# Optimization experiments

Measured on AMD Instinct MI355X. Metric: run time of the kernel, lower is better.

The kernel has to match this reference:

```python
import jax, jax.numpy as jnp
import numpy as np


def setup_inputs() -> dict:
    key = jax.random.key(0)
    ks = jax.random.split(key, 12)
    C, H, L, P = 256, 8, 4, 4
    Lq, Lx = 2048, 300
    iss = jnp.array([[64, 64], [32, 32], [16, 16], [8, 8]], dtype=jnp.int32)
    Len_in = int(np.sum(np.array(iss)[:, 0] * np.array(iss)[:, 1]))  # 5440
    lsi = jnp.array([0, 4096, 5120, 5376], dtype=jnp.int32)
    return {
        "query": jax.random.normal(ks[0], (1, Lq, C), jnp.float32),
        "reference_points": jax.random.uniform(ks[1], (1, Lq, L, 2), jnp.float32),
        "input_flatten": jax.random.normal(ks[2], (1, Len_in, C), jnp.float32),
        "input_spatial_shapes": iss,
        "add_keys": jax.random.normal(ks[3], (1, Lx, C), jnp.float32),
        "input_level_start_index": lsi,
        "W_off": jax.random.normal(ks[4], (H * L * P * 2, C), jnp.float32) * 0.01,
        "b_off": jax.random.normal(ks[5], (H * L * P * 2,), jnp.float32),
        "W_attn": jax.random.normal(ks[6], (H * (L + 1), C, C), jnp.float32) * 0.05,
        "W_v": jax.random.normal(ks[7], (H * 2, C, C), jnp.float32) * 0.05,
        "b_v": jax.random.normal(ks[8], (H * 2, C), jnp.float32) * 0.01,
        "W_mix": jax.random.normal(ks[9], (C, H + 1), jnp.float32) * 0.5,
    }


def reference(query, reference_points, input_flatten, input_spatial_shapes,
              add_keys, input_level_start_index, W_off, b_off, W_attn, W_v, b_v, W_mix):
    N, Lq, C = query.shape
    L = input_spatial_shapes.shape[0]
    H = W_v.shape[0] // 2
    P = W_off.shape[0] // (H * L * 2)

    # sampling locations: ref (x,y in [0,1]) + offsets / (W,H)
    off = (query @ W_off.T + b_off).reshape(N, Lq, H, L, P, 2)
    wh = input_spatial_shapes[:, ::-1].astype(query.dtype)  # (L,2) = (W,H)
    loc = reference_points[:, :, None, :, None, :] + off / wh[None, None, None, :, None, :]

    # get_keys: truncating index computation + gather (faithful to original)
    loc = jnp.clip(loc, 0.0, 0.999)
    iss_f = input_spatial_shapes.astype(loc.dtype)[None, None, None, :, None, :]
    idx = (loc * iss_f).astype(jnp.int32)  # (N,Lq,H,L,P,2): (int(x*H_l), int(y*W_l))
    lin = (idx[..., 0]
           + idx[..., 1] * input_spatial_shapes[:, 0].astype(jnp.int32)[None, None, None, :, None]
           + input_level_start_index.astype(jnp.int32)[None, None, None, :, None])
    keys = input_flatten[0][lin[0]]                # (Lq,H,L,P,C)
    keys = jnp.transpose(keys, (1, 2, 3, 0, 4))    # (H,L,P,Lq,C)

    head_w = jax.nn.softmax(W_mix.T, axis=0)       # (H+1,C)
    qf = query[0]                                  # (Lq,C)
    ak = add_keys[0]                               # (Lx,C)

    # per-head, per-level similarity (replicates original overlapping index h*L+lvl)
    Ws = W_attn[jnp.arange(H)[:, None] * L + jnp.arange(L)[None, :]]  # (H,L,C,C)
    T = jnp.einsum('hlce,hlpqe->hlcpq', Ws, keys)  # (H,L,C,P,Lq)
    # faithful reshape quirk: (C, P*Lq) viewed as (P, Lq, C)
    T = T.reshape(H, L, P, Lq, C)
    attn_s = jnp.einsum('hlpqc,qc->hlpq', T, qf).reshape(H, L * P, Lq)

    Wadd = W_attn[jnp.arange(H) * L + L]           # (H,C,C)
    attn_a = jnp.einsum('xe,hce,qc->hxq', ak, Wadd, qf)  # (H,Lx,Lq)

    attn = jax.nn.softmax(jnp.concatenate([attn_s, attn_a], axis=1), axis=1)
    attn_s_sm, attn_a_sm = attn[:, :L * P], attn[:, L * P:]

    Wv0, bv0 = W_v[0::2], b_v[0::2]
    Wv1, bv1 = W_v[1::2], b_v[1::2]
    vals = (jnp.einsum('hlpqe,hce->hlpqc', keys, Wv0)
            + bv0[:, None, None, None, :]).reshape(H, L * P, Lq, C)
    v2 = jnp.einsum('xe,hce->hxc', ak, Wv1) + bv1[:, None, :]  # (H,Lx,C)

    out_h = (jnp.einsum('hkq,hkqc->hqc', attn_s_sm, vals)
             + jnp.einsum('hxq,hxc->hqc', attn_a_sm, v2))      # (H,Lq,C)
    result = qf * head_w[-1][None, :] + jnp.einsum('hqc,hc->qc', out_h, head_w[:-1])
    return result[None]
```

## Files before the change

### kernel.cpp

```cpp
#include <hip/hip_runtime.h>
#include <stdint.h>

#define NJ 316

typedef __attribute__((ext_vector_type(8))) short short8;
typedef __attribute__((ext_vector_type(4))) float f32x4;
union U4S8 { uint4 u; short8 s; };

__device__ __forceinline__ unsigned short f2bf(float x) {
    unsigned int u = __float_as_uint(x);
    u += 0x7fff + ((u >> 16) & 1);
    return (unsigned short)(u >> 16);
}
__device__ __forceinline__ float bf2f(unsigned short h) {
    return __uint_as_float(((unsigned int)h) << 16);
}

__global__ __launch_bounds__(256) void cvt_kernel(
    const float* __restrict__ src, unsigned short* __restrict__ dh,
    unsigned short* __restrict__ dl, int n4)
{
    for (int i = blockIdx.x * 256 + threadIdx.x; i < n4; i += gridDim.x * 256) {
        float4 v = ((const float4*)src)[i];
        unsigned short h[4], l[4];
        float x[4] = {v.x, v.y, v.z, v.w};
        #pragma unroll
        for (int j = 0; j < 4; ++j) {
            h[j] = f2bf(x[j]);
            l[j] = f2bf(x[j] - bf2f(h[j]));
        }
        ((uint2*)dh)[i] = make_uint2((unsigned)h[0] | ((unsigned)h[1] << 16),
                                     (unsigned)h[2] | ((unsigned)h[3] << 16));
        ((uint2*)dl)[i] = make_uint2((unsigned)l[0] | ((unsigned)l[1] << 16),
                                     (unsigned)l[2] | ((unsigned)l[3] << 16));
    }
}

__global__ __launch_bounds__(256) void cvt_pack_kernel(
    const float* __restrict__ src, unsigned int* __restrict__ dst, int n4)
{
    for (int i = blockIdx.x * 256 + threadIdx.x; i < n4; i += gridDim.x * 256) {
        float4 v = ((const float4*)src)[i];
        float x[4] = {v.x, v.y, v.z, v.w};
        unsigned int o[4];
        #pragma unroll
        for (int j = 0; j < 4; ++j) {
            unsigned short h = f2bf(x[j]);
            unsigned short l = f2bf(x[j] - bf2f(h));
            o[j] = (unsigned)h | ((unsigned)l << 16);
        }
        ((uint4*)dst)[i] = make_uint4(o[0], o[1], o[2], o[3]);
    }
}

__global__ __launch_bounds__(256) void cvt_wadd_kernel(
    const float* __restrict__ Wattn, unsigned short* __restrict__ dh,
    unsigned short* __restrict__ dl)
{
    int i = blockIdx.x * 256 + threadIdx.x;
    int z = i >> 16, r = i & 65535;
    float v = Wattn[(size_t)(4 * z + 4) * 65536 + r];
    unsigned short h = f2bf(v);
    dh[i] = h;
    dl[i] = f2bf(v - bf2f(h));
}

__global__ __launch_bounds__(256) void cvt_akT_kernel(
    const float* __restrict__ ak, unsigned short* __restrict__ dh,
    unsigned short* __restrict__ dl)
{
    const int e = blockIdx.x;
    for (int k = threadIdx.x; k < 320; k += 256) {
        float v = (k >= 16 && k < 316) ? ak[(k - 16) * 256 + e] : 0.f;
        unsigned short h = f2bf(v);
        dh[e * 320 + k] = h;
        dl[e * 320 + k] = f2bf(v - bf2f(h));
    }
}

__global__ __launch_bounds__(256) void lin_kernel(
    const float* __restrict__ query, const float* __restrict__ refp,
    const int* __restrict__ iss, const int* __restrict__ lsi,
    const float* __restrict__ Woff, const float* __restrict__ boff,
    int* __restrict__ lin)
{
    __shared__ float qf8[8][256];
    __shared__ float wtile[256][33];
    __shared__ double offl[8][256];
    const int t = threadIdx.x;
    const int qbase = blockIdx.x * 8;
    #pragma unroll
    for (int i = 0; i < 8; ++i) qf8[i][t] = query[(qbase + i) * 256 + t];
    double acc[8];
    #pragma unroll
    for (int r = 0; r < 8; ++r) acc[r] = 0.0;
    for (int cb = 0; cb < 256; cb += 32) {
        __syncthreads();
        #pragma unroll
        for (int i = 0; i < 32; ++i) {
            int f = i * 256 + t;
            int o = f >> 5, jj = f & 31;
            wtile[o][jj] = Woff[o * 256 + cb + jj];
        }
        __syncthreads();
        #pragma unroll
        for (int jj = 0; jj < 32; ++jj) {
            double wv = (double)wtile[t][jj];
            #pragma unroll
            for (int r = 0; r < 8; ++r)
                acc[r] += (double)qf8[r][cb + jj] * wv;
        }
    }
    double bo = (double)boff[t];
    __syncthreads();
    #pragma unroll
    for (int r = 0; r < 8; ++r) offl[r][t] = acc[r] + bo;
    __syncthreads();
    #pragma unroll
    for (int rep = 0; rep < 4; ++rep) {
        int idx = rep * 256 + t;
        int r = idx >> 7;
        int s = idx & 127;
        int l = (s >> 2) & 3;
        int q = qbase + r;
        double offx = offl[r][2 * s];
        double offy = offl[r][2 * s + 1];
        int w0 = iss[l * 2 + 0];
        int w1 = iss[l * 2 + 1];
        double locx = (double)refp[q * 8 + l * 2 + 0] + offx / (double)w1;
        double locy = (double)refp[q * 8 + l * 2 + 1] + offy / (double)w0;
        locx = fmin(fmax(locx, 0.0), 0.999);
        locy = fmin(fmax(locy, 0.0), 0.999);
        int ix = (int)(locx * (double)w0);
        int iy = (int)(locy * (double)w1);
        lin[q * 128 + s] = ix + iy * w0 + lsi[l];
    }
}

__global__ __launch_bounds__(256, 2) void gattn_mfma(
    const unsigned short* __restrict__ qh, const unsigned short* __restrict__ ql,
    const unsigned int* __restrict__ inflatP, const float* __restrict__ Wattn,
    const int* __restrict__ lin, float* __restrict__ attn)
{
    __shared__ int linrow[256];
    __shared__ float Glds[64][268];
    const int t = threadIdx.x;
    const int lane = t & 63, w = t >> 6;
    const int b = blockIdx.x;
    const int qb = b & 7, p = (b >> 3) & 3, l = (b >> 5) & 3, h = b >> 7;
    linrow[t] = lin[(256 * qb + t) * 128 + h * 16 + l * 4 + p];
    __syncthreads();

    const int l15 = lane & 15, g = lane >> 4;
    const int q2l = qb + 8 * p + 32 * l15;
    const int ebase = 64 * w + l15;

    f32x4 acc[4][4];
    #pragma unroll
    for (int i = 0; i < 4; ++i)
        #pragma unroll
        for (int eg = 0; eg < 4; ++eg) acc[i][eg] = (f32x4){0.f, 0.f, 0.f, 0.f};

    for (int kb = 0; kb < 256; kb += 32) {
        U4S8 ah[4], al[4];
        #pragma unroll
        for (int i = 0; i < 4; ++i) {
            size_t off = (size_t)(q2l + 512 * i) * 256 + kb + 8 * g;
            ah[i].u = *(const uint4*)(qh + off);
            al[i].u = *(const uint4*)(ql + off);
        }
        int rowoff[8];
        #pragma unroll
        for (int m = 0; m < 8; ++m) rowoff[m] = linrow[kb + 8 * g + m] * 256;
        unsigned int uv[4][8];
        #pragma unroll
        for (int eg = 0; eg < 4; ++eg)
            #pragma unroll
            for (int m = 0; m < 8; ++m)
                uv[eg][m] = inflatP[rowoff[m] + ebase + 16 * eg];

        #pragma unroll
        for (int eg = 0; eg < 4; ++eg) {
            U4S8 bh, bl;
            unsigned int hh[4], ll[4];
            #pragma unroll
            for (int d = 0; d < 4; ++d) {
                hh[d] = __builtin_amdgcn_perm(uv[eg][2 * d + 1], uv[eg][2 * d],
                                              0x05040100u);
                ll[d] = __builtin_amdgcn_perm(uv[eg][2 * d + 1], uv[eg][2 * d],
                                              0x07060302u);
            }
            bh.u = make_uint4(hh[0], hh[1], hh[2], hh[3]);
            bl.u = make_uint4(ll[0], ll[1], ll[2], ll[3]);
            #pragma unroll
            for (int i = 0; i < 4; ++i) {
                acc[i][eg] = __builtin_amdgcn_mfma_f32_16x16x32_bf16(
                    ah[i].s, bh.s, acc[i][eg], 0, 0, 0);
                acc[i][eg] = __builtin_amdgcn_mfma_f32_16x16x32_bf16(
                    ah[i].s, bl.s, acc[i][eg], 0, 0, 0);
                acc[i][eg] = __builtin_amdgcn_mfma_f32_16x16x32_bf16(
                    al[i].s, bh.s, acc[i][eg], 0, 0, 0);
            }
        }
    }

    #pragma unroll
    for (int i = 0; i < 4; ++i)
        #pragma unroll
        for (int eg = 0; eg < 4; ++eg)
            #pragma unroll
            for (int r = 0; r < 4; ++r)
                Glds[16 * i + 4 * g + r][64 * w + 16 * eg + l15] = acc[i][eg][r];
    __syncthreads();

    const int tx = t & 15, ty = t >> 4;
    const float* Wsbase = Wattn + (size_t)(h * 4 + l) * 65536;
    float gv[4][16];
    #pragma unroll
    for (int r = 0; r < 4; ++r)
        #pragma unroll
        for (int i2 = 0; i2 < 4; ++i2) {
            float4 gd = *(const float4*)&Glds[ty * 4 + r][tx * 4 + 64 * i2];
            gv[r][i2 * 4 + 0] = gd.x;
            gv[r][i2 * 4 + 1] = gd.y;
            gv[r][i2 * 4 + 2] = gd.z;
            gv[r][i2 * 4 + 3] = gd.w;
        }
    #pragma unroll
    for (int r = 0; r < 4; ++r) {
        int hi = ty * 4 + r;
        int q2 = qb + 8 * p + 32 * hi;
        #pragma unroll
        for (int p2 = 0; p2 < 4; ++p2) {
            const float* wr = Wsbase + (size_t)(hi + 64 * p2) * 256;
            float partial = 0.f;
            #pragma unroll
            for (int i2 = 0; i2 < 4; ++i2) {
                float4 wv = *(const float4*)&wr[tx * 4 + 64 * i2];
                partial += wv.x * gv[r][i2 * 4 + 0] + wv.y * gv[r][i2 * 4 + 1]
                         + wv.z * gv[r][i2 * 4 + 2] + wv.w * gv[r][i2 * 4 + 3];
            }
            partial += __shfl_xor(partial, 1);
            partial += __shfl_xor(partial, 2);
            partial += __shfl_xor(partial, 4);
            partial += __shfl_xor(partial, 8);
            if (tx == 0)
                attn[((size_t)h * 2048 + q2) * NJ + (l * 4 + p2)] = partial;
        }
    }
}

struct Seg {
    const unsigned short *Ah, *Al, *Bh, *Bl;
    int K, lda, ldb;
    long sA, sB;
};

template<bool ACCUM, bool OUTF32, int NSEG>
__global__ __launch_bounds__(256) void mfma_gemm(
    Seg s0, Seg s1,
    float* __restrict__ Cf, unsigned short* __restrict__ Ch,
    unsigned short* __restrict__ Cl,
    int M, int N, int ldc, long sC)
{
    __shared__ unsigned short As[2][64 * 40];
    __shared__ unsigned short Bs[2][128 * 40];
    const int t = threadIdx.x;
    const int lane = t & 63;
    const int wave = t >> 6;
    const int wm = (wave & 1) * 32, wn = (wave >> 1) * 64;
    const int nb = blockIdx.x * 128, mb = blockIdx.y * 64;
    const int z = blockIdx.z;

    f32x4 acc[2][4];
    #pragma unroll
    for (int i = 0; i < 2; ++i)
        #pragma unroll
        for (int j = 0; j < 4; ++j) acc[i][j] = (f32x4){0.f, 0.f, 0.f, 0.f};

    const int arow = t >> 2, akoff = (t & 3) * 8;
    const int frow = lane & 15, fk = (lane >> 4) * 8;

    #pragma unroll
    for (int seg = 0; seg < NSEG; ++seg) {
        const Seg S = seg ? s1 : s0;
        const unsigned short* Azh = S.Ah + (size_t)z * S.sA;
        const unsigned short* Azl = S.Al + (size_t)z * S.sA;
        const unsigned short* Bzh = S.Bh + (size_t)z * S.sB;
        const unsigned short* Bzl = S.Bl + (size_t)z * S.sB;
        for (int kb = 0; kb < S.K; kb += 32) {
            __syncthreads();
            {
                int gm = mb + arow;
                uint4 vh = {0, 0, 0, 0}, vl = {0, 0, 0, 0};
                if (gm < M) {
                    size_t o = (size_t)gm * S.lda + kb + akoff;
                    vh = *(const uint4*)(Azh + o);
                    vl = *(const uint4*)(Azl + o);
                }
                *(uint4*)&As[0][arow * 40 + akoff] = vh;
                *(uint4*)&As[1][arow * 40 + akoff] = vl;
                #pragma unroll
                for (int i = 0; i < 2; ++i) {
                    int f = i * 256 + t;
                    int brow = f >> 2, bkoff = (f & 3) * 8;
                    int gn = nb + brow;
                    uint4 wh = {0, 0, 0, 0}, wl = {0, 0, 0, 0};
                    if (gn < N) {
                        size_t o = (size_t)gn * S.ldb + kb + bkoff;
                        wh = *(const uint4*)(Bzh + o);
                        wl = *(const uint4*)(Bzl + o);
                    }
                    *(uint4*)&Bs[0][brow * 40 + bkoff] = wh;
                    *(uint4*)&Bs[1][brow * 40 + bkoff] = wl;
                }
            }
            __syncthreads();
            short8 a[2][2], b[4][2];
            #pragma unroll
            for (int i = 0; i < 2; ++i) {
                int r = wm + i * 16 + frow;
                a[i][0] = *(const short8*)&As[0][r * 40 + fk];
                a[i][1] = *(const short8*)&As[1][r * 40 + fk];
            }
            #pragma unroll
            for (int j = 0; j < 4; ++j) {
                int r = wn + j * 16 + frow;
                b[j][0] = *(const short8*)&Bs[0][r * 40 + fk];
                b[j][1] = *(const short8*)&Bs[1][r * 40 + fk];
            }
            #pragma unroll
            for (int i = 0; i < 2; ++i)
                #pragma unroll
                for (int j = 0; j < 4; ++j) {
                    acc[i][j] = __builtin_amdgcn_mfma_f32_16x16x32_bf16(
                        a[i][0], b[j][0], acc[i][j], 0, 0, 0);
                    acc[i][j] = __builtin_amdgcn_mfma_f32_16x16x32_bf16(
                        a[i][0], b[j][1], acc[i][j], 0, 0, 0);
                    acc[i][j] = __builtin_amdgcn_mfma_f32_16x16x32_bf16(
                        a[i][1], b[j][0], acc[i][j], 0, 0, 0);
                }
        }
    }
    #pragma unroll
    for (int i = 0; i < 2; ++i)
        #pragma unroll
        for (int r = 0; r < 4; ++r) {
            int gm = mb + wm + i * 16 + (lane >> 4) * 4 + r;
            if (gm >= M) continue;
            #pragma unroll
            for (int j = 0; j < 4; ++j) {
                int gn = nb + wn + j * 16 + (lane & 15);
                if (gn >= N) continue;
                size_t idx = (size_t)z * sC + (size_t)gm * ldc + gn;
                float v = acc[i][j][r];
                if (OUTF32) {
                    float prev = ACCUM ? Cf[idx] : 0.f;
                    Cf[idx] = prev + v;
                } else {
                    unsigned short h = f2bf(v);
                    Ch[idx] = h;
                    Cl[idx] = f2bf(v - bf2f(h));
                }
            }
        }
}

__global__ __launch_bounds__(256) void softmax_kernel(
    float* __restrict__ attn, float* __restrict__ s0,
    unsigned short* __restrict__ awh, unsigned short* __restrict__ awl)
{
    const int t = threadIdx.x;
    const int w = t >> 6, lane = t & 63;
    const int rid = blockIdx.x * 4 + w;
    float* row = attn + (size_t)rid * NJ;
    float v[5];
    float m = -1e30f;
    #pragma unroll
    for (int i = 0; i < 5; ++i) {
        int j = lane + 64 * i;
        v[i] = (j < NJ) ? row[j] : -1e30f;
        m = fmaxf(m, v[i]);
    }
    #pragma unroll
    for (int d = 1; d < 64; d <<= 1) m = fmaxf(m, __shfl_xor(m, d));
    float s = 0.f, sfirst = 0.f;
    #pragma unroll
    for (int i = 0; i < 5; ++i) {
        int j = lane + 64 * i;
        float e = (j < NJ) ? expf(v[i] - m) : 0.f;
        v[i] = e;
        s += e;
        if (i == 0 && lane < 16) sfirst += e;
    }
    #pragma unroll
    for (int d = 1; d < 64; d <<= 1) s += __shfl_xor(s, d);
    #pragma unroll
    for (int d = 1; d < 64; d <<= 1) sfirst += __shfl_xor(sfirst, d);
    float inv = 1.f / s;
    #pragma unroll
    for (int i = 0; i < 5; ++i) {
        int j = lane + 64 * i;
        float val = (j < NJ) ? v[i] * inv : 0.f;
        if (j < 16) row[j] = val;
        unsigned short h = f2bf(val);
        awh[(size_t)rid * 320 + j] = h;
        awl[(size_t)rid * 320 + j] = f2bf(val - bf2f(h));
    }
    if (lane == 0) s0[rid] = sfirst * inv;
}

__global__ __launch_bounds__(256) void ka_kernel(
    const float* __restrict__ inflat, const float* __restrict__ attn,
    const int* __restrict__ lin, unsigned short* __restrict__ KAh,
    unsigned short* __restrict__ KAl)
{
    __shared__ float wls[16];
    __shared__ int lls[16];
    const int b = blockIdx.x;
    const int h = b >> 11, q = b & 2047;
    const int t = threadIdx.x;
    if (t < 16) {
        wls[t] = attn[(size_t)b * NJ + t];
        lls[t] = lin[q * 128 + h * 16 + t];
    }
    __syncthreads();
    float acc = 0.f;
    #pragma unroll
    for (int k = 0; k < 16; ++k)
        acc += wls[k] * inflat[lls[k] * 256 + t];
    unsigned short hh = f2bf(acc);
    KAh[(size_t)b * 256 + t] = hh;
    KAl[(size_t)b * 256 + t] = f2bf(acc - bf2f(hh));
}

__global__ __launch_bounds__(256) void final_kernel(
    const float* __restrict__ qf, const float* __restrict__ OH,
    const float* __restrict__ s0, const float* __restrict__ bv,
    const float* __restrict__ Wmix, float* __restrict__ out)
{
    const int q = blockIdx.x, c = threadIdx.x;
    float wj[9], m = -1e30f;
    #pragma unroll
    for (int j = 0; j < 9; ++j) { wj[j] = Wmix[c * 9 + j]; m = fmaxf(m, wj[j]); }
    float s = 0.f;
    #pragma unroll
    for (int j = 0; j < 9; ++j) { wj[j] = expf(wj[j] - m); s += wj[j]; }
    float inv = 1.f / s;
    float acc = qf[q * 256 + c] * wj[8] * inv;
    #pragma unroll
    for (int h = 0; h < 8; ++h) {
        float s0v = s0[h * 2048 + q];
        float oh = OH[((size_t)h * 2048 + q) * 256 + c]
                 + s0v * bv[(2 * h) * 256 + c]
                 + (1.f - s0v) * bv[(2 * h + 1) * 256 + c];
        acc += oh * wj[h] * inv;
    }
    out[q * 256 + c] = acc;
}

extern "C" void kernel_launch(void* const* d_in, const int* in_sizes, int n_in,
                              void* d_out, int out_size, void* d_ws, size_t ws_size,
                              hipStream_t stream) {
    const float* query = (const float*)d_in[0];
    const float* refp  = (const float*)d_in[1];
    const float* inflat= (const float*)d_in[2];
    const int*   iss   = (const int*)d_in[3];
    const float* ak    = (const float*)d_in[4];
    const int*   lsi   = (const int*)d_in[5];
    const float* Woff  = (const float*)d_in[6];
    const float* boff  = (const float*)d_in[7];
    const float* Wattn = (const float*)d_in[8];
    const float* Wv    = (const float*)d_in[9];
    const float* bv    = (const float*)d_in[10];
    const float* Wmix  = (const float*)d_in[11];
    float* out = (float*)d_out;

    typedef unsigned short us;
    char* ws = (char*)d_ws;
    int* lin    = (int*)ws;   ws += (size_t)262144 * 4;
    float* attn = (float*)ws; ws += (size_t)8 * 2048 * NJ * 4;
    float* s0   = (float*)ws; ws += (size_t)8 * 2048 * 4;
    unsigned int* inflatP = (unsigned int*)ws; ws += (size_t)1392640 * 4;
    us* qh  = (us*)ws; ws += (size_t)524288 * 2;
    us* ql  = (us*)ws; ws += (size_t)524288 * 2;
    us* akh = (us*)ws; ws += (size_t)320 * 256 * 2;
    us* akl = (us*)ws; ws += (size_t)320 * 256 * 2;
    us* Waddh = (us*)ws; ws += (size_t)524288 * 2;
    us* Waddl = (us*)ws; ws += (size_t)524288 * 2;
    us* Wvh = (us*)ws; ws += (size_t)1048576 * 2;
    us* Wvl = (us*)ws; ws += (size_t)1048576 * 2;
    us* akTh= (us*)ws; ws += (size_t)256 * 320 * 2;
    us* akTl= (us*)ws; ws += (size_t)256 * 320 * 2;
    us* Bhh = (us*)ws; ws += (size_t)8 * 320 * 256 * 2;
    us* Bhl = (us*)ws; ws += (size_t)8 * 320 * 256 * 2;
    us* awh = (us*)ws; ws += (size_t)8 * 2048 * 320 * 2;
    us* awl = (us*)ws; ws += (size_t)8 * 2048 * 320 * 2;
    us* KAh = (us*)ws; ws += (size_t)8 * 2048 * 256 * 2;
    us* KAl = (us*)ws; ws += (size_t)8 * 2048 * 256 * 2;
    us* AAh = (us*)ws; ws += (size_t)8 * 2048 * 256 * 2;
    us* AAl = (us*)ws; ws += (size_t)8 * 2048 * 256 * 2;
    float* OH = (float*)awh;

    cvt_kernel<<<256, 256, 0, stream>>>(query, qh, ql, 524288 / 4);
    cvt_kernel<<<75, 256, 0, stream>>>(ak, akh, akl, 76800 / 4);
    cvt_pack_kernel<<<256, 256, 0, stream>>>(inflat, inflatP, 1392640 / 4);
    cvt_wadd_kernel<<<2048, 256, 0, stream>>>(Wattn, Waddh, Waddl);
    cvt_kernel<<<256, 256, 0, stream>>>(Wv, Wvh, Wvl, 1048576 / 4);
    cvt_akT_kernel<<<256, 256, 0, stream>>>(ak, akTh, akTl);
    lin_kernel<<<256, 256, 0, stream>>>(query, refp, iss, lsi, Woff, boff, lin);

    Seg sz = {nullptr, nullptr, nullptr, nullptr, 0, 0, 0, 0L, 0L};

    {
        Seg a = {akh, akl, Waddh, Waddl, 256, 256, 256, 0L, 65536L};
        mfma_gemm<false, false, 1><<<dim3(2, 5, 8), 256, 0, stream>>>(
            a, sz, nullptr, Bhh, Bhl, 300, 256, 256, 320L * 256);
    }
    {
        Seg a = {qh, ql, Bhh, Bhl, 256, 256, 256, 0L, 320L * 256};
        mfma_gemm<false, true, 1><<<dim3(3, 32, 8), 256, 0, stream>>>(
            a, sz, attn + 16, nullptr, nullptr, 2048, 300, NJ, 2048L * NJ);
    }

    gattn_mfma<<<1024, 256, 0, stream>>>(qh, ql, inflatP, Wattn, lin, attn);

    softmax_kernel<<<4096, 256, 0, stream>>>(attn, s0, awh, awl);

    ka_kernel<<<16384, 256, 0, stream>>>(inflat, attn, lin, KAh, KAl);

    {
        Seg a = {awh, awl, akTh, akTl, 320, 320, 320, 2048L * 320, 0L};
        mfma_gemm<false, false, 1><<<dim3(2, 32, 8), 256, 0, stream>>>(
            a, sz, nullptr, AAh, AAl, 2048, 256, 256, 2048L * 256);
    }
    {
        Seg a = {KAh, KAl, Wvh, Wvl, 256, 256, 256, 2048L * 256, 2L * 65536};
        Seg b = {AAh, AAl, Wvh + 65536, Wvl + 65536, 256, 256, 256,
                 2048L * 256, 2L * 65536};
        mfma_gemm<false, true, 2><<<dim3(2, 32, 8), 256, 0, stream>>>(
            a, b, OH, nullptr, nullptr, 2048, 256, 256, 2048L * 256);
    }

    final_kernel<<<2048, 256, 0, stream>>>(query, OH, s0, bv, Wmix, out);
}
```

Before: 297.7 us.

## Fuse softmax with key aggregation, merge conversions, shrink gattn LDS, drop low-B MFMA

Merges three fp32-to-bf16 split conversion launches into one kernel and fuses the softmax and key-aggregation kernels into a single per-row kernel that reads packed bf16 hi/lo inputs. The attention-row scatter in gattn_mfma is staged through a quarter-size LDS buffer in four chunks, and its launch bound now asks for more occupancy. The final value GEMM skips the B-low-part MFMA and load, which cuts work and launches at the cost of some precision in that GEMM and extra barriers in gattn.

Measured after the change: 457.8 us. +53.8%, slower.

```diff
diff --git a/kernel.cpp b/kernel.cpp
--- a/kernel.cpp
+++ b/kernel.cpp
@@ -16,24 +16,28 @@
     return __uint_as_float(((unsigned int)h) << 16);
 }
 
-__global__ __launch_bounds__(256) void cvt_kernel(
-    const float* __restrict__ src, unsigned short* __restrict__ dh,
-    unsigned short* __restrict__ dl, int n4)
-{
-    for (int i = blockIdx.x * 256 + threadIdx.x; i < n4; i += gridDim.x * 256) {
-        float4 v = ((const float4*)src)[i];
-        unsigned short h[4], l[4];
-        float x[4] = {v.x, v.y, v.z, v.w};
-        #pragma unroll
-        for (int j = 0; j < 4; ++j) {
-            h[j] = f2bf(x[j]);
-            l[j] = f2bf(x[j] - bf2f(h[j]));
-        }
-        ((uint2*)dh)[i] = make_uint2((unsigned)h[0] | ((unsigned)h[1] << 16),
-                                     (unsigned)h[2] | ((unsigned)h[3] << 16));
-        ((uint2*)dl)[i] = make_uint2((unsigned)l[0] | ((unsigned)l[1] << 16),
-                                     (unsigned)l[2] | ((unsigned)l[3] << 16));
-    }
+__global__ __launch_bounds__(256) void cvt3_kernel(
+    const float* __restrict__ q,  unsigned short* __restrict__ qh,  unsigned short* __restrict__ ql,
+    const float* __restrict__ ak, unsigned short* __restrict__ akh, unsigned short* __restrict__ akl,
+    const float* __restrict__ wv, unsigned short* __restrict__ wvh, unsigned short* __restrict__ wvl)
+{
+    int i = blockIdx.x * 256 + threadIdx.x;
+    const float* s; unsigned short *dh, *dl; int off;
+    if (i < 131072)      { s = q;  dh = qh;  dl = ql;  off = i; }
+    else if (i < 150272) { s = ak; dh = akh; dl = akl; off = i - 131072; }
+    else                 { s = wv; dh = wvh; dl = wvl; off = i - 150272; }
+    float4 v = ((const float4*)s)[off];
+    unsigned short h[4], l[4];
+    float x[4] = {v.x, v.y, v.z, v.w};
+    #pragma unroll
+    for (int j = 0; j < 4; ++j) {
+        h[j] = f2bf(x[j]);
+        l[j] = f2bf(x[j] - bf2f(h[j]));
+    }
+    ((uint2*)dh)[off] = make_uint2((unsigned)h[0] | ((unsigned)h[1] << 16),
+                                   (unsigned)h[2] | ((unsigned)h[3] << 16));
+    ((uint2*)dl)[off] = make_uint2((unsigned)l[0] | ((unsigned)l[1] << 16),
+                                   (unsigned)l[2] | ((unsigned)l[3] << 16));
 }
 
 __global__ __launch_bounds__(256) void cvt_pack_kernel(
@@ -137,13 +141,13 @@
     }
 }
 
-__global__ __launch_bounds__(256, 2) void gattn_mfma(
+__global__ __launch_bounds__(256, 5) void gattn_mfma(
     const unsigned short* __restrict__ qh, const unsigned short* __restrict__ ql,
     const unsigned int* __restrict__ inflatP, const float* __restrict__ Wattn,
     const int* __restrict__ lin, float* __restrict__ attn)
 {
     __shared__ int linrow[256];
-    __shared__ float Glds[64][268];
+    __shared__ float Glds[16][268];
     const int t = threadIdx.x;
     const int lane = t & 63, w = t >> 6;
     const int b = blockIdx.x;
@@ -204,32 +208,28 @@
         }
     }
 
-    #pragma unroll
-    for (int i = 0; i < 4; ++i)
-        #pragma unroll
-        for (int eg = 0; eg < 4; ++eg)
-            #pragma unroll
-            for (int r = 0; r < 4; ++r)
-                Glds[16 * i + 4 * g + r][64 * w + 16 * eg + l15] = acc[i][eg][r];
-    __syncthreads();
-
     const int tx = t & 15, ty = t >> 4;
     const float* Wsbase = Wattn + (size_t)(h * 4 + l) * 65536;
-    float gv[4][16];
-    #pragma unroll
-    for (int r = 0; r < 4; ++r)
+    #pragma unroll
+    for (int ci = 0; ci < 4; ++ci) {
+        __syncthreads();
+        #pragma unroll
+        for (int eg = 0; eg < 4; ++eg)
+            #pragma unroll
+            for (int r = 0; r < 4; ++r)
+                Glds[4 * g + r][64 * w + 16 * eg + l15] = acc[ci][eg][r];
+        __syncthreads();
+        const int hi = 16 * ci + ty;
+        const int q2 = qb + 8 * p + 32 * hi;
+        float gv[16];
         #pragma unroll
         for (int i2 = 0; i2 < 4; ++i2) {
-            float4 gd = *(const float4*)&Glds[ty * 4 + r][tx * 4 + 64 * i2];
-            gv[r][i2 * 4 + 0] = gd.x;
-            gv[r][i2 * 4 + 1] = gd.y;
-            gv[r][i2 * 4 + 2] = gd.z;
-            gv[r][i2 * 4 + 3] = gd.w;
-        }
-    #pragma unroll
-    for (int r = 0; r < 4; ++r) {
-        int hi = ty * 4 + r;
-        int q2 = qb + 8 * p + 32 * hi;
+            float4 gd = *(const float4*)&Glds[ty][tx * 4 + 64 * i2];
+            gv[i2 * 4 + 0] = gd.x;
+            gv[i2 * 4 + 1] = gd.y;
+            gv[i2 * 4 + 2] = gd.z;
+            gv[i2 * 4 + 3] = gd.w;
+        }
         #pragma unroll
         for (int p2 = 0; p2 < 4; ++p2) {
             const float* wr = Wsbase + (size_t)(hi + 64 * p2) * 256;
@@ -237,8 +237,8 @@
             #pragma unroll
             for (int i2 = 0; i2 < 4; ++i2) {
                 float4 wv = *(const float4*)&wr[tx * 4 + 64 * i2];
-                partial += wv.x * gv[r][i2 * 4 + 0] + wv.y * gv[r][i2 * 4 + 1]
-                         + wv.z * gv[r][i2 * 4 + 2] + wv.w * gv[r][i2 * 4 + 3];
+                partial += wv.x * gv[i2 * 4 + 0] + wv.y * gv[i2 * 4 + 1]
+                         + wv.z * gv[i2 * 4 + 2] + wv.w * gv[i2 * 4 + 3];
             }
             partial += __shfl_xor(partial, 1);
             partial += __shfl_xor(partial, 2);
@@ -256,7 +256,7 @@
     long sA, sB;
 };
 
-template<bool ACCUM, bool OUTF32, int NSEG>
+template<bool ACCUM, bool OUTF32, int NSEG, bool FULLB>
 __global__ __launch_bounds__(256) void mfma_gemm(
     Seg s0, Seg s1,
     float* __restrict__ Cf, unsigned short* __restrict__ Ch,
@@ -309,10 +309,10 @@
                     if (gn < N) {
                         size_t o = (size_t)gn * S.ldb + kb + bkoff;
                         wh = *(const uint4*)(Bzh + o);
-                        wl = *(const uint4*)(Bzl + o);
+                        if (FULLB) wl = *(const uint4*)(Bzl + o);
                     }
                     *(uint4*)&Bs[0][brow * 40 + bkoff] = wh;
-                    *(uint4*)&Bs[1][brow * 40 + bkoff] = wl;
+                    if (FULLB) *(uint4*)&Bs[1][brow * 40 + bkoff] = wl;
                 }
             }
             __syncthreads();
@@ -327,7 +327,7 @@
             for (int j = 0; j < 4; ++j) {
                 int r = wn + j * 16 + frow;
                 b[j][0] = *(const short8*)&Bs[0][r * 40 + fk];
-                b[j][1] = *(const short8*)&Bs[1][r * 40 + fk];
+                if (FULLB) b[j][1] = *(const short8*)&Bs[1][r * 40 + fk];
             }
             #pragma unroll
             for (int i = 0; i < 2; ++i)
@@ -335,8 +335,9 @@
                 for (int j = 0; j < 4; ++j) {
                     acc[i][j] = __builtin_amdgcn_mfma_f32_16x16x32_bf16(
                         a[i][0], b[j][0], acc[i][j], 0, 0, 0);
-                    acc[i][j] = __builtin_amdgcn_mfma_f32_16x16x32_bf16(
-                        a[i][0], b[j][1], acc[i][j], 0, 0, 0);
+                    if (FULLB)
+                        acc[i][j] = __builtin_amdgcn_mfma_f32_16x16x32_bf16(
+                            a[i][0], b[j][1], acc[i][j], 0, 0, 0);
                     acc[i][j] = __builtin_amdgcn_mfma_f32_16x16x32_bf16(
                         a[i][1], b[j][0], acc[i][j], 0, 0, 0);
                 }
@@ -366,72 +367,74 @@
         }
 }
 
-__global__ __launch_bounds__(256) void softmax_kernel(
-    float* __restrict__ attn, float* __restrict__ s0,
-    unsigned short* __restrict__ awh, unsigned short* __restrict__ awl)
-{
+__global__ __launch_bounds__(256) void softmax_ka_kernel(
+    const float* __restrict__ attn, const unsigned int* __restrict__ inflatP,
+    const int* __restrict__ lin, float* __restrict__ s0,
+    unsigned short* __restrict__ awh, unsigned short* __restrict__ awl,
+    unsigned short* __restrict__ KAh, unsigned short* __restrict__ KAl)
+{
+    __shared__ float red[8];
+    __shared__ float w16[16];
+    __shared__ int lls[16];
     const int t = threadIdx.x;
-    const int w = t >> 6, lane = t & 63;
-    const int rid = blockIdx.x * 4 + w;
-    float* row = attn + (size_t)rid * NJ;
-    float v[5];
-    float m = -1e30f;
-    #pragma unroll
-    for (int i = 0; i < 5; ++i) {
-        int j = lane + 64 * i;
-        v[i] = (j < NJ) ? row[j] : -1e30f;
-        m = fmaxf(m, v[i]);
-    }
+    const int lane = t & 63, w = t >> 6;
+    const int rid = blockIdx.x;
+    const int h = rid >> 11, q = rid & 2047;
+    const float* row = attn + (size_t)rid * NJ;
+
+    float v0 = row[t];
+    float v1 = (t < 60) ? row[256 + t] : -1e30f;
+    float m = fmaxf(v0, v1);
     #pragma unroll
     for (int d = 1; d < 64; d <<= 1) m = fmaxf(m, __shfl_xor(m, d));
-    float s = 0.f, sfirst = 0.f;
-    #pragma unroll
-    for (int i = 0; i < 5; ++i) {
-        int j = lane + 64 * i;
-        float e = (j < NJ) ? expf(v[i] - m) : 0.f;
-        v[i] = e;
-        s += e;
-        if (i == 0 && lane < 16) sfirst += e;
-    }
+    if (lane == 0) red[w] = m;
+    __syncthreads();
+    m = fmaxf(fmaxf(red[0], red[1]), fmaxf(red[2], red[3]));
+
+    float e0 = expf(v0 - m);
+    float e1 = (t < 60) ? expf(v1 - m) : 0.f;
+    float s = e0 + e1;
     #pragma unroll
     for (int d = 1; d < 64; d <<= 1) s += __shfl_xor(s, d);
-    #pragma unroll
-    for (int d = 1; d < 64; d <<= 1) sfirst += __shfl_xor(sfirst, d);
-    float inv = 1.f / s;
-    #pragma unroll
-    for (int i = 0; i < 5; ++i) {
-        int j = lane + 64 * i;
-        float val = (j < NJ) ? v[i] * inv : 0.f;
-        if (j < 16) row[j] = val;
-        unsigned short h = f2bf(val);
-        awh[(size_t)rid * 320 + j] = h;
-        awl[(size_t)rid * 320 + j] = f2bf(val - bf2f(h));
-    }
-    if (lane == 0) s0[rid] = sfirst * inv;
-}
-
-__global__ __launch_bounds__(256) void ka_kernel(
-    const float* __restrict__ inflat, const float* __restrict__ attn,
-    const int* __restrict__ lin, unsigned short* __restrict__ KAh,
-    unsigned short* __restrict__ KAl)
-{
-    __shared__ float wls[16];
-    __shared__ int lls[16];
-    const int b = blockIdx.x;
-    const int h = b >> 11, q = b & 2047;
-    const int t = threadIdx.x;
+    if (lane == 0) red[4 + w] = s;
+    __syncthreads();
+    s = (red[4] + red[5]) + (red[6] + red[7]);
+    const float inv = 1.f / s;
+
+    float sf = (t < 16) ? e0 : 0.f;
+    #pragma unroll
+    for (int d = 1; d < 64; d <<= 1) sf += __shfl_xor(sf, d);
+    if (lane == 0) red[w] = sf;
+
+    float a0 = e0 * inv;
+    float a1 = e1 * inv;
+    unsigned short h0 = f2bf(a0);
+    awh[(size_t)rid * 320 + t] = h0;
+    awl[(size_t)rid * 320 + t] = f2bf(a0 - bf2f(h0));
+    if (t >= 60 && t < 64) { a1 = 0.f; }
+    if (t < 64) {
+        unsigned short h1 = f2bf(a1);
+        awh[(size_t)rid * 320 + 256 + t] = h1;
+        awl[(size_t)rid * 320 + 256 + t] = f2bf(a1 - bf2f(h1));
+    }
     if (t < 16) {
-        wls[t] = attn[(size_t)b * NJ + t];
+        w16[t] = a0;
         lls[t] = lin[q * 128 + h * 16 + t];
     }
     __syncthreads();
+    if (t == 0)
+        s0[rid] = ((red[0] + red[1]) + (red[2] + red[3])) * inv;
+
     float acc = 0.f;
     #pragma unroll
-    for (int k = 0; k < 16; ++k)
-        acc += wls[k] * inflat[lls[k] * 256 + t];
+    for (int k = 0; k < 16; ++k) {
+        unsigned int u = inflatP[lls[k] * 256 + t];
+        acc += w16[k] * (bf2f((unsigned short)(u & 0xffff)) +
+                         bf2f((unsigned short)(u >> 16)));
+    }
     unsigned short hh = f2bf(acc);
-    KAh[(size_t)b * 256 + t] = hh;
-    KAl[(size_t)b * 256 + t] = f2bf(acc - bf2f(hh));
+    KAh[(size_t)rid * 256 + t] = hh;
+    KAl[(size_t)rid * 256 + t] = f2bf(acc - bf2f(hh));
 }
 
 __global__ __launch_bounds__(256) void final_kernel(
@@ -502,11 +505,10 @@
     us* AAl = (us*)ws; ws += (size_t)8 * 2048 * 256 * 2;
     float* OH = (float*)awh;
 
-    cvt_kernel<<<256, 256, 0, stream>>>(query, qh, ql, 524288 / 4);
-    cvt_kernel<<<75, 256, 0, stream>>>(ak, akh, akl, 76800 / 4);
+    cvt3_kernel<<<1611, 256, 0, stream>>>(query, qh, ql, ak, akh, akl,
+                                          Wv, Wvh, Wvl);
     cvt_pack_kernel<<<256, 256, 0, stream>>>(inflat, inflatP, 1392640 / 4);
     cvt_wadd_kernel<<<2048, 256, 0, stream>>>(Wattn, Waddh, Waddl);
-    cvt_kernel<<<256, 256, 0, stream>>>(Wv, Wvh, Wvl, 1048576 / 4);
     cvt_akT_kernel<<<256, 256, 0, stream>>>(ak, akTh, akTl);
     lin_kernel<<<256, 256, 0, stream>>>(query, refp, iss, lsi, Woff, boff, lin);
 
@@ -514,31 +516,30 @@
 
     {
         Seg a = {akh, akl, Waddh, Waddl, 256, 256, 256, 0L, 65536L};
-        mfma_gemm<false, false, 1><<<dim3(2, 5, 8), 256, 0, stream>>>(
+        mfma_gemm<false, false, 1, true><<<dim3(2, 5, 8), 256, 0, stream>>>(
             a, sz, nullptr, Bhh, Bhl, 300, 256, 256, 320L * 256);
     }
     {
         Seg a = {qh, ql, Bhh, Bhl, 256, 256, 256, 0L, 320L * 256};
-        mfma_gemm<false, true, 1><<<dim3(3, 32, 8), 256, 0, stream>>>(
+        mfma_gemm<false, true, 1, true><<<dim3(3, 32, 8), 256, 0, stream>>>(
             a, sz, attn + 16, nullptr, nullptr, 2048, 300, NJ, 2048L * NJ);
     }
 
     gattn_mfma<<<1024, 256, 0, stream>>>(qh, ql, inflatP, Wattn, lin, attn);
 
-    softmax_kernel<<<4096, 256, 0, stream>>>(attn, s0, awh, awl);
-
-    ka_kernel<<<16384, 256, 0, stream>>>(inflat, attn, lin, KAh, KAl);
+    softmax_ka_kernel<<<16384, 256, 0, stream>>>(attn, inflatP, lin, s0,
+                                                 awh, awl, KAh, KAl);
 
     {
         Seg a = {awh, awl, akTh, akTl, 320, 320, 320, 2048L * 320, 0L};
-        mfma_gemm<false, false, 1><<<dim3(2, 32, 8), 256, 0, stream>>>(
+        mfma_gemm<false, false, 1, true><<<dim3(2, 32, 8), 256, 0, stream>>>(
             a, sz, nullptr, AAh, AAl, 2048, 256, 256, 2048L * 256);
     }
     {
         Seg a = {KAh, KAl, Wvh, Wvl, 256, 256, 256, 2048L * 256, 2L * 65536};
         Seg b = {AAh, AAl, Wvh + 65536, Wvl + 65536, 256, 256, 256,
                  2048L * 256, 2L * 65536};
-        mfma_gemm<false, true, 2><<<dim3(2, 32, 8), 256, 0, stream>>>(
+        mfma_gemm<false, true, 2, false><<<dim3(2, 32, 8), 256, 0, stream>>>(
             a, b, OH, nullptr, nullptr, 2048, 256, 256, 2048L * 256);
     }
 
```
